# Optimization experiments

Measured on AMD Instinct MI355X. Metric: run time of the kernel, lower is better.

Reference implementation:

```python
import jax, jax.numpy as jnp
import numpy as np

N = 100000
E = 1600000
IN_CH = 128
HID = 32
HEADS = 4
OUT_CH = 32
NEG_SLOPE = 0.2


def _gat_layer(x, W, a_src, a_dst, b, src, dst, heads, out_ch):
    """PyG-style GATConv (concat=True). x: [N, F_in]; returns [N, heads*out_ch]."""
    n = x.shape[0]
    h = (x @ W).reshape(n, heads, out_ch)                    # [N, H, C]
    alpha_s = jnp.einsum('nhc,hc->nh', h, a_src)             # [N, H]
    alpha_d = jnp.einsum('nhc,hc->nh', h, a_dst)             # [N, H]
    logits = jax.nn.leaky_relu(alpha_s[src] + alpha_d[dst], NEG_SLOPE)  # [E, H]
    # segment softmax over destination node
    m = jax.ops.segment_max(logits, dst, num_segments=n)
    m = jnp.where(jnp.isfinite(m), m, 0.0)
    p = jnp.exp(logits - m[dst])
    denom = jax.ops.segment_sum(p, dst, num_segments=n)
    alpha = p / (denom[dst] + 1e-16)                         # [E, H]
    msg = h[src] * alpha[..., None]                          # [E, H, C]
    out = jax.ops.segment_sum(msg, dst, num_segments=n)      # [N, H, C]
    return out.reshape(n, heads * out_ch) + b


def setup_inputs() -> dict:
    key = jax.random.key(0)
    ks = jax.random.split(key, 16)
    x = jax.random.normal(ks[0], (N, IN_CH), dtype=jnp.float32)
    edge_index = jax.random.randint(ks[1], (2, E), 0, N, dtype=jnp.int32)

    def glorot(k, shape):
        fan = shape[0] + shape[-1]
        return jax.random.normal(k, shape, dtype=jnp.float32) * np.sqrt(2.0 / fan)

    hid = HID * HEADS  # 128
    return {
        'x': x,
        'edge_index': edge_index,
        'W1': glorot(ks[2], (IN_CH, hid)),
        'a_src1': glorot(ks[3], (HEADS, HID)),
        'a_dst1': glorot(ks[4], (HEADS, HID)),
        'b1': jnp.zeros((hid,), jnp.float32),
        'W2': glorot(ks[5], (hid, hid)),
        'a_src2': glorot(ks[6], (HEADS, HID)),
        'a_dst2': glorot(ks[7], (HEADS, HID)),
        'b2': jnp.zeros((hid,), jnp.float32),
        'W3': glorot(ks[8], (hid, OUT_CH)),
        'a_src3': glorot(ks[9], (1, OUT_CH)),
        'a_dst3': glorot(ks[10], (1, OUT_CH)),
        'b3': jnp.zeros((OUT_CH,), jnp.float32),
    }


def reference(x, edge_index, W1, a_src1, a_dst1, b1, W2, a_src2, a_dst2, b2,
              W3, a_src3, a_dst3, b3):
    # add self-loops (PyG GATConv default add_self_loops=True)
    loop = jnp.arange(N, dtype=edge_index.dtype)
    src = jnp.concatenate([edge_index[0], loop])
    dst = jnp.concatenate([edge_index[1], loop])

    h = _gat_layer(x, W1, a_src1, a_dst1, b1, src, dst, HEADS, HID)
    h = jax.nn.elu(h)
    h = _gat_layer(h, W2, a_src2, a_dst2, b2, src, dst, HEADS, HID)
    h = jax.nn.elu(h)
    out = _gat_layer(h, W3, a_src3, a_dst3, b3, src, dst, 1, OUT_CH)
    return out
```

## Files before the change

kernel.cpp:

```cpp
#include <hip/hip_runtime.h>
#include <cstdint>

#define NN 100000
#define EE 1600000
#define ET (EE + NN)
#define NBUCK 782
#define BCAP 3584

typedef unsigned int u32;
typedef unsigned short u16;
typedef short bf16x8 __attribute__((ext_vector_type(8)));
typedef float f32x4 __attribute__((ext_vector_type(4)));

__device__ __forceinline__ u16 f2bf(float f) {
    union { float f; u32 i; } v; v.f = f;
    u32 r = v.i + 0x7FFFu + ((v.i >> 16) & 1u);
    return (u16)(r >> 16);
}
__device__ __forceinline__ float bf2f(u32 u) {
    union { u32 i; float f; } v; v.i = u << 16; return v.f;
}
__device__ __forceinline__ void get_edge(const int* __restrict__ ei, int e, int& s, int& d) {
    if (e < EE) { s = ei[e]; d = ei[EE + e]; }
    else { s = e - EE; d = s; }
}
__device__ __forceinline__ float leaky(float x) { return x > 0.f ? x : 0.2f * x; }

__global__ __launch_bounds__(256) void wprep_kernel(
    const float* __restrict__ W1, const float* __restrict__ W2, const float* __restrict__ W3,
    u16* __restrict__ wt1, u16* __restrict__ wt2, u16* __restrict__ wt3)
{
    int i = blockIdx.x * 256 + threadIdx.x;
    if (i < 16384)      { int c = i >> 7, k = i & 127; wt1[i] = f2bf(W1[k * 128 + c]); }
    else if (i < 32768) { int j = i - 16384; int c = j >> 7, k = j & 127; wt2[j] = f2bf(W2[k * 128 + c]); }
    else if (i < 36864) { int j = i - 32768; int c = j >> 7, k = j & 127; wt3[j] = f2bf(W3[k * 32 + c]); }
}

template<int OUTC, bool IN16>
__global__ __launch_bounds__(256) void gemm_mfma(
    const void* __restrict__ Xv, const u16* __restrict__ Wt16g,
    const float* __restrict__ asw, const float* __restrict__ adw,
    u16* __restrict__ Hout16, float* __restrict__ as_o, float* __restrict__ ad_o)
{
    constexpr int NT = OUTC / 16;
    constexpr int LDSU = (OUTC == 128) ? 13056 : 6528;
    constexpr int HS = (OUTC == 128) ? 132 : 36;
    __shared__ u32 lds[LDSU];
    u32* wl = lds + 64 * 68;

    const int tid = threadIdx.x;
    const int r0 = blockIdx.x * 64;

    if (IN16) {
        const u32* Xg = (const u32*)Xv;
        for (int i = tid; i < 64 * 64; i += 256) {
            int r = i >> 6, k2 = i & 63;
            u32 v = 0;
            if (r0 + r < NN) v = Xg[(size_t)(r0 + r) * 64 + k2];
            lds[r * 68 + k2] = v;
        }
    } else {
        const float* Xf = (const float*)Xv;
        for (int i = tid; i < 64 * 64; i += 256) {
            int r = i >> 6, k2 = i & 63;
            u32 v = 0;
            if (r0 + r < NN) {
                float2 f = *(const float2*)(Xf + (size_t)(r0 + r) * 128 + k2 * 2);
                v = (u32)f2bf(f.x) | ((u32)f2bf(f.y) << 16);
            }
            lds[r * 68 + k2] = v;
        }
    }
    {
        const u32* Wg = (const u32*)Wt16g;
        for (int i = tid; i < OUTC * 64; i += 256) {
            int c = i >> 6, k2 = i & 63;
            wl[c * 68 + k2] = Wg[i];
        }
    }
    __syncthreads();

    const int w = tid >> 6, l = tid & 63;
    const int lm = l & 15, q = l >> 4;

    f32x4 acc[NT];
    #pragma unroll
    for (int T = 0; T < NT; T++)
        #pragma unroll
        for (int r = 0; r < 4; r++) acc[T][r] = 0.f;

    #pragma unroll
    for (int kc = 0; kc < 4; kc++) {
        bf16x8 af = *(const bf16x8*)&lds[(16 * w + lm) * 68 + kc * 16 + q * 4];
        #pragma unroll
        for (int T = 0; T < NT; T++) {
            bf16x8 bfr = *(const bf16x8*)&wl[(16 * T + lm) * 68 + kc * 16 + q * 4];
            acc[T] = __builtin_amdgcn_mfma_f32_16x16x32_bf16(af, bfr, acc[T], 0, 0, 0);
        }
    }
    __syncthreads();

    float* hl = (float*)lds;
    #pragma unroll
    for (int T = 0; T < NT; T++)
        #pragma unroll
        for (int rg = 0; rg < 4; rg++)
            hl[(16 * w + q * 4 + rg) * HS + 16 * T + lm] = acc[T][rg];
    __syncthreads();

    for (int i = tid; i < 64 * (OUTC / 2); i += 256) {
        int r = i / (OUTC / 2), k2 = i % (OUTC / 2);
        int row = r0 + r;
        if (row < NN) {
            float a = hl[r * HS + k2 * 2];
            float b = hl[r * HS + k2 * 2 + 1];
            ((u32*)Hout16)[(size_t)row * (OUTC / 2) + k2] = (u32)f2bf(a) | ((u32)f2bf(b) << 16);
        }
    }
    if (OUTC == 128) {
        const int row = tid >> 2, part = tid & 3;
        const float* hp = &hl[row * HS + part * 32];
        const float* aw = asw + part * 32;
        const float* dw = adw + part * 32;
        float s = 0.f, d = 0.f;
        #pragma unroll
        for (int c = 0; c < 32; c++) { float hv = hp[c]; s += hv * aw[c]; d += hv * dw[c]; }
        const int grow = r0 + row;
        if (grow < NN) { as_o[(size_t)grow * 4 + part] = s; ad_o[(size_t)grow * 4 + part] = d; }
    } else {
        if (tid < 64) {
            const float* hp = &hl[tid * HS];
            float s = 0.f, d = 0.f;
            #pragma unroll
            for (int c = 0; c < 32; c++) { float hv = hp[c]; s += hv * asw[c]; d += hv * adw[c]; }
            const int grow = r0 + tid;
            if (grow < NN) { as_o[grow] = s; ad_o[grow] = d; }
        }
    }
}

__global__ __launch_bounds__(256) void bin_fill_kernel(const int* __restrict__ ei,
    int* __restrict__ gcur, u32* __restrict__ pairs)
{
    __shared__ int hist[NBUCK];
    __shared__ int base[NBUCK];
    const int t = threadIdx.x;
    for (int i = t; i < NBUCK; i += 256) hist[i] = 0;
    __syncthreads();
    const int chunk = (ET + gridDim.x - 1) / gridDim.x;
    const int e0 = blockIdx.x * chunk;
    const int e1 = min(e0 + chunk, ET);
    for (int e = e0 + t; e < e1; e += 256) {
        int s, d; get_edge(ei, e, s, d);
        atomicAdd(&hist[d >> 7], 1);
    }
    __syncthreads();
    for (int i = t; i < NBUCK; i += 256) {
        int c = hist[i];
        base[i] = c ? atomicAdd(&gcur[i], c) : 0;
        hist[i] = 0;
    }
    __syncthreads();
    for (int e = e0 + t; e < e1; e += 256) {
        int s, d; get_edge(ei, e, s, d);
        int b = d >> 7;
        int pos = atomicAdd(&hist[b], 1);
        pairs[(size_t)b * BCAP + base[b] + pos] = ((u32)(d & 127) << 25) | (u32)s;
    }
}

__global__ __launch_bounds__(1024) void bscan_kernel(const int* __restrict__ bcnt,
    int* __restrict__ bbase, int* __restrict__ rowp)
{
    __shared__ int lds[1024];
    const int t = threadIdx.x;
    int v = (t < NBUCK) ? bcnt[t] : 0;
    lds[t] = v;
    __syncthreads();
    for (int off = 1; off < 1024; off <<= 1) {
        int x = (t >= off) ? lds[t - off] : 0;
        __syncthreads();
        lds[t] += x;
        __syncthreads();
    }
    if (t < NBUCK) bbase[t] = lds[t] - v;
    if (t == 0) { bbase[NBUCK] = ET; rowp[NN] = ET; }
}

__global__ __launch_bounds__(256) void bucket_csr_kernel(const u32* __restrict__ pairs,
    const int* __restrict__ bcnt, const int* __restrict__ bbase,
    int* __restrict__ rowp, int* __restrict__ col)
{
    __shared__ int hist[128], scn[128];
    __shared__ int col_lds[BCAP];
    const int b = blockIdx.x;
    const int cbase = bbase[b];
    const int cnt = bcnt[b];
    const u32* pk0 = pairs + (size_t)b * BCAP;
    const int t = threadIdx.x;
    if (t < 128) hist[t] = 0;
    __syncthreads();
    for (int i = t; i < cnt; i += 256)
        atomicAdd(&hist[pk0[i] >> 25], 1);
    __syncthreads();
    if (t < 128) scn[t] = hist[t];
    __syncthreads();
    for (int off = 1; off < 128; off <<= 1) {
        int x = (t < 128 && t >= off) ? scn[t - off] : 0;
        __syncthreads();
        if (t < 128) scn[t] += x;
        __syncthreads();
    }
    if (t < 128) {
        int ex = scn[t] - hist[t];
        int node = b * 128 + t;
        if (node < NN) rowp[node] = cbase + ex;
        hist[t] = ex;
    }
    __syncthreads();
    for (int i = t; i < cnt; i += 256) {
        u32 pk = pk0[i];
        int pos = atomicAdd(&hist[pk >> 25], 1);
        if (pos < BCAP) col_lds[pos] = pk & 0x1FFFFFFu;
    }
    __syncthreads();
    for (int i = t; i < cnt; i += 256)
        col[cbase + i] = col_lds[i];
}

template<bool DOELU>
__global__ __launch_bounds__(256) void agg4_kernel(
    const int* __restrict__ rowp, const int* __restrict__ col,
    const float* __restrict__ as_, const float* __restrict__ ad_,
    const u16* __restrict__ Hb16, const float* __restrict__ bias,
    u16* __restrict__ outp16)
{
    const int lane = threadIdx.x & 63;
    const int node = blockIdx.x * 4 + (threadIdx.x >> 6);
    const int sub = lane & 15;
    const int h = lane >> 4;

    const int start = rowp[node];
    const int end   = rowp[node + 1];
    const float adv = ad_[(size_t)node * 4 + h];
    const char* hbase = (const char*)Hb16 + lane * 4;
    const float2 bv = *(const float2*)(bias + lane * 2);

    float m = -1e30f, den = 0.f, a0 = 0.f, a1 = 0.f;
    for (int j0 = start; j0 < end; j0 += 16) {
        const int j = j0 + sub;
        const bool valid = (j < end);
        const int s = valid ? col[j] : 0;
        const float lg = valid ? leaky(as_[(size_t)s * 4 + h] + adv) : -1e30f;
        float cm = lg;
        #pragma unroll
        for (int off = 8; off; off >>= 1) cm = fmaxf(cm, __shfl_xor(cm, off));
        const float mnew = fmaxf(m, cm);
        const float sc = __expf(m - mnew);
        a0 *= sc; a1 *= sc; den *= sc; m = mnew;
        const float p = valid ? __expf(lg - m) : 0.f;
        float ps = p;
        #pragma unroll
        for (int off = 8; off; off >>= 1) ps += __shfl_xor(ps, off);
        den += ps;
        const int soff = s << 8;
        int so[16]; float pi[16];
        #pragma unroll
        for (int i = 0; i < 16; i++) {
            so[i] = __shfl(soff, i);
            pi[i] = __shfl(p, (h << 4) | i);
        }
        #pragma unroll
        for (int i = 0; i < 16; i++) {
            u32 wv = *(const u32*)(hbase + so[i]);
            a0 += pi[i] * bf2f(wv & 0xffffu);
            a1 += pi[i] * bf2f(wv >> 16);
        }
    }
    const float rden = 1.f / (den + 1e-16f);
    float v0 = a0 * rden + bv.x;
    float v1 = a1 * rden + bv.y;
    if (DOELU) {
        v0 = v0 > 0.f ? v0 : (__expf(v0) - 1.f);
        v1 = v1 > 0.f ? v1 : (__expf(v1) - 1.f);
    }
    u32 pack = (u32)f2bf(v0) | ((u32)f2bf(v1) << 16);
    *(u32*)(outp16 + (size_t)node * 128 + lane * 2) = pack;
}

__global__ __launch_bounds__(256) void agg1_kernel(
    const int* __restrict__ rowp, const int* __restrict__ col,
    const float* __restrict__ as_, const float* __restrict__ ad_,
    const u16* __restrict__ Hb16, const float* __restrict__ bias,
    float* __restrict__ outp)
{
    const int t = threadIdx.x;
    const int lane = t & 31;
    const int node = blockIdx.x * 8 + (t >> 5);

    const int start = rowp[node];
    const int end   = rowp[node + 1];
    const float adv = ad_[node];
    const char* hbase = (const char*)Hb16 + lane * 2;
    const float bvv = bias[lane];

    float m = -1e30f, den = 0.f, acc = 0.f;
    for (int j0 = start; j0 < end; j0 += 32) {
        const int j = j0 + lane;
        const bool valid = (j < end);
        const int s = valid ? col[j] : 0;
        const float lg = valid ? leaky(as_[s] + adv) : -1e30f;
        float cm = lg;
        #pragma unroll
        for (int off = 16; off; off >>= 1) cm = fmaxf(cm, __shfl_xor(cm, off, 32));
        const float mnew = fmaxf(m, cm);
        const float sc = __expf(m - mnew);
        acc *= sc; den *= sc; m = mnew;
        const float p = valid ? __expf(lg - m) : 0.f;
        float ps = p;
        #pragma unroll
        for (int off = 16; off; off >>= 1) ps += __shfl_xor(ps, off, 32);
        den += ps;
        const int soff = s << 6;
        int so[32]; float pi[32];
        #pragma unroll
        for (int i = 0; i < 32; i++) {
            so[i] = __shfl(soff, i, 32);
            pi[i] = __shfl(p, i, 32);
        }
        #pragma unroll
        for (int i = 0; i < 32; i++)
            acc += pi[i] * bf2f((u32)*(const u16*)(hbase + so[i]));
    }
    outp[(size_t)node * 32 + lane] = acc / (den + 1e-16f) + bvv;
}

extern "C" void kernel_launch(void* const* d_in, const int* in_sizes, int n_in,
                              void* d_out, int out_size, void* d_ws, size_t ws_size,
                              hipStream_t stream)
{
    const float* x   = (const float*)d_in[0];
    const int*   ei  = (const int*)d_in[1];
    const float* W1  = (const float*)d_in[2];
    const float* as1 = (const float*)d_in[3];
    const float* ad1 = (const float*)d_in[4];
    const float* b1  = (const float*)d_in[5];
    const float* W2  = (const float*)d_in[6];
    const float* as2 = (const float*)d_in[7];
    const float* ad2 = (const float*)d_in[8];
    const float* b2  = (const float*)d_in[9];
    const float* W3  = (const float*)d_in[10];
    const float* as3 = (const float*)d_in[11];
    const float* ad3 = (const float*)d_in[12];
    const float* b3  = (const float*)d_in[13];
    float* outp = (float*)d_out;

    char* ws = (char*)d_ws;
    u16*   hb16  = (u16*)(ws);
    u16*   xb16  = (u16*)(ws + 25700000);
    u16*   h3b16 = (u16*)(ws + 51400000);
    float* asb   = (float*)(ws + 57900000);
    float* adb   = (float*)(ws + 59500000);
    int*   rowp  = (int*)(ws + 61100000);
    int*   col   = (int*)(ws + 61600000);
    u32*   pairs = (u32*)(ws + 68400032);
    int*   gcur  = (int*)(ws + 79700000);
    int*   bbase = (int*)(ws + 79704096);
    u16*   wt1   = (u16*)(ws + 79710000);
    u16*   wt2   = (u16*)(ws + 79750000);
    u16*   wt3   = (u16*)(ws + 79790000);

    const dim3 B(256);
    const int gG = (NN + 63) / 64;

    wprep_kernel<<<144, B, 0, stream>>>(W1, W2, W3, wt1, wt2, wt3);
    hipMemsetAsync(gcur, 0, NBUCK * 4, stream);
    bin_fill_kernel<<<256, B, 0, stream>>>(ei, gcur, pairs);
    bscan_kernel<<<1, dim3(1024), 0, stream>>>(gcur, bbase, rowp);
    bucket_csr_kernel<<<NBUCK, B, 0, stream>>>(pairs, gcur, bbase, rowp, col);

    gemm_mfma<128, false><<<gG, B, 0, stream>>>(x, wt1, as1, ad1, hb16, asb, adb);
    agg4_kernel<true><<<NN / 4, B, 0, stream>>>(rowp, col, asb, adb, hb16, b1, xb16);

    gemm_mfma<128, true><<<gG, B, 0, stream>>>(xb16, wt2, as2, ad2, hb16, asb, adb);
    agg4_kernel<true><<<NN / 4, B, 0, stream>>>(rowp, col, asb, adb, hb16, b2, xb16);

    gemm_mfma<32, true><<<gG, B, 0, stream>>>(xb16, wt3, as3, ad3, h3b16, asb, adb);
    agg1_kernel<<<NN / 8, B, 0, stream>>>(rowp, col, asb, adb, h3b16, b3, outp);
}
```

Baseline: 454.3 us.

## Replace shuffle broadcasts with DPP reductions, LDS staging, readlane and exp2

The GEMM now stores attention logits pre-scaled by log2(e), so the aggregation kernels can use exp2f instead of __expf. The 16-lane max and sum reductions use DPP row rotations instead of xor shuffles. The per-edge weight broadcast moves from ds_bpermute shuffles into a per-wave LDS buffer read back as vectors, and source offsets are broadcast with readlane. The goal is to cut cross-lane instruction overhead in the gather loops. It relies on wave-local LDS ordering enforced only by a waitcnt, with no barrier.

Measured after the change: 473.8 us. 4.3% more time.

```diff
diff --git a/kernel.cpp b/kernel.cpp
--- a/kernel.cpp
+++ b/kernel.cpp
@@ -6,11 +6,13 @@
 #define ET (EE + NN)
 #define NBUCK 782
 #define BCAP 3584
+#define LOG2E 1.4426950408889634f
 
 typedef unsigned int u32;
 typedef unsigned short u16;
 typedef short bf16x8 __attribute__((ext_vector_type(8)));
 typedef float f32x4 __attribute__((ext_vector_type(4)));
+typedef int i32x4 __attribute__((ext_vector_type(4)));
 
 __device__ __forceinline__ u16 f2bf(float f) {
     union { float f; u32 i; } v; v.f = f;
@@ -25,6 +27,22 @@
     else { s = e - EE; d = s; }
 }
 __device__ __forceinline__ float leaky(float x) { return x > 0.f ? x : 0.2f * x; }
+
+#define DPP_ROR_F(x, CTRL) __int_as_float(__builtin_amdgcn_update_dpp(0, __float_as_int(x), (CTRL), 0xF, 0xF, true))
+__device__ __forceinline__ float rmax16(float x) {
+    x = fmaxf(x, DPP_ROR_F(x, 0x121));
+    x = fmaxf(x, DPP_ROR_F(x, 0x122));
+    x = fmaxf(x, DPP_ROR_F(x, 0x124));
+    x = fmaxf(x, DPP_ROR_F(x, 0x128));
+    return x;
+}
+__device__ __forceinline__ float rsum16(float x) {
+    x += DPP_ROR_F(x, 0x121);
+    x += DPP_ROR_F(x, 0x122);
+    x += DPP_ROR_F(x, 0x124);
+    x += DPP_ROR_F(x, 0x128);
+    return x;
+}
 
 __global__ __launch_bounds__(256) void wprep_kernel(
     const float* __restrict__ W1, const float* __restrict__ W2, const float* __restrict__ W3,
@@ -126,7 +144,10 @@
         #pragma unroll
         for (int c = 0; c < 32; c++) { float hv = hp[c]; s += hv * aw[c]; d += hv * dw[c]; }
         const int grow = r0 + row;
-        if (grow < NN) { as_o[(size_t)grow * 4 + part] = s; ad_o[(size_t)grow * 4 + part] = d; }
+        if (grow < NN) {
+            as_o[(size_t)grow * 4 + part] = s * LOG2E;
+            ad_o[(size_t)grow * 4 + part] = d * LOG2E;
+        }
     } else {
         if (tid < 64) {
             const float* hp = &hl[tid * HS];
@@ -134,7 +155,10 @@
             #pragma unroll
             for (int c = 0; c < 32; c++) { float hv = hp[c]; s += hv * asw[c]; d += hv * adw[c]; }
             const int grow = r0 + tid;
-            if (grow < NN) { as_o[grow] = s; ad_o[grow] = d; }
+            if (grow < NN) {
+                as_o[grow] = s * LOG2E;
+                ad_o[grow] = d * LOG2E;
+            }
         }
     }
 }
@@ -235,15 +259,18 @@
     const u16* __restrict__ Hb16, const float* __restrict__ bias,
     u16* __restrict__ outp16)
 {
-    const int lane = threadIdx.x & 63;
-    const int node = blockIdx.x * 4 + (threadIdx.x >> 6);
+    __shared__ float pst[4][64];
+    const int tid = threadIdx.x;
+    const int w = tid >> 6;
+    const int lane = tid & 63;
+    const int node = blockIdx.x * 4 + w;
     const int sub = lane & 15;
     const int h = lane >> 4;
 
     const int start = rowp[node];
     const int end   = rowp[node + 1];
     const float adv = ad_[(size_t)node * 4 + h];
-    const char* hbase = (const char*)Hb16 + lane * 4;
+    const int lane4 = lane << 2;
     const float2 bv = *(const float2*)(bias + lane * 2);
 
     float m = -1e30f, den = 0.f, a0 = 0.f, a1 = 0.f;
@@ -252,29 +279,27 @@
         const bool valid = (j < end);
         const int s = valid ? col[j] : 0;
         const float lg = valid ? leaky(as_[(size_t)s * 4 + h] + adv) : -1e30f;
-        float cm = lg;
-        #pragma unroll
-        for (int off = 8; off; off >>= 1) cm = fmaxf(cm, __shfl_xor(cm, off));
+        const float cm = rmax16(lg);
         const float mnew = fmaxf(m, cm);
-        const float sc = __expf(m - mnew);
+        const float sc = exp2f(m - mnew);
         a0 *= sc; a1 *= sc; den *= sc; m = mnew;
-        const float p = valid ? __expf(lg - m) : 0.f;
-        float ps = p;
-        #pragma unroll
-        for (int off = 8; off; off >>= 1) ps += __shfl_xor(ps, off);
-        den += ps;
-        const int soff = s << 8;
-        int so[16]; float pi[16];
+        const float p = valid ? exp2f(lg - m) : 0.f;
+        pst[w][lane] = p;
+        den += rsum16(p);
+        const u32 soff = (u32)s << 8;
+        asm volatile("s_waitcnt lgkmcnt(0)" ::: "memory");
+        const f32x4 pv0 = *(const f32x4*)&pst[w][h * 16 + 0];
+        const f32x4 pv1 = *(const f32x4*)&pst[w][h * 16 + 4];
+        const f32x4 pv2 = *(const f32x4*)&pst[w][h * 16 + 8];
+        const f32x4 pv3 = *(const f32x4*)&pst[w][h * 16 + 12];
         #pragma unroll
         for (int i = 0; i < 16; i++) {
-            so[i] = __shfl(soff, i);
-            pi[i] = __shfl(p, (h << 4) | i);
-        }
-        #pragma unroll
-        for (int i = 0; i < 16; i++) {
-            u32 wv = *(const u32*)(hbase + so[i]);
-            a0 += pi[i] * bf2f(wv & 0xffffu);
-            a1 += pi[i] * bf2f(wv >> 16);
+            const int so = __builtin_amdgcn_readlane((int)soff, i);
+            const char* rp = (const char*)Hb16 + so;
+            const u32 wv = *(const u32*)(rp + lane4);
+            const float pi = (i < 4 ? pv0 : i < 8 ? pv1 : i < 12 ? pv2 : pv3)[i & 3];
+            a0 += pi * bf2f(wv & 0xffffu);
+            a1 += pi * bf2f(wv >> 16);
         }
     }
     const float rden = 1.f / (den + 1e-16f);
@@ -294,45 +319,61 @@
     const u16* __restrict__ Hb16, const float* __restrict__ bias,
     float* __restrict__ outp)
 {
+    __shared__ float pst[4][64];
+    __shared__ int   sst[4][64];
     const int t = threadIdx.x;
-    const int lane = t & 31;
+    const int w = t >> 6;
+    const int lane = t & 63;
+    const int l32 = lane & 31;
+    const int half = lane >> 5;
     const int node = blockIdx.x * 8 + (t >> 5);
 
     const int start = rowp[node];
     const int end   = rowp[node + 1];
     const float adv = ad_[node];
-    const char* hbase = (const char*)Hb16 + lane * 2;
-    const float bvv = bias[lane];
+    const char* hb = (const char*)Hb16;
+    const int l2 = l32 << 1;
+    const float bvv = bias[l32];
 
     float m = -1e30f, den = 0.f, acc = 0.f;
     for (int j0 = start; j0 < end; j0 += 32) {
-        const int j = j0 + lane;
+        const int j = j0 + l32;
         const bool valid = (j < end);
         const int s = valid ? col[j] : 0;
         const float lg = valid ? leaky(as_[s] + adv) : -1e30f;
-        float cm = lg;
-        #pragma unroll
-        for (int off = 16; off; off >>= 1) cm = fmaxf(cm, __shfl_xor(cm, off, 32));
+        float cm = rmax16(lg);
+        cm = fmaxf(cm, __shfl_xor(cm, 16, 32));
         const float mnew = fmaxf(m, cm);
-        const float sc = __expf(m - mnew);
+        const float sc = exp2f(m - mnew);
         acc *= sc; den *= sc; m = mnew;
-        const float p = valid ? __expf(lg - m) : 0.f;
-        float ps = p;
-        #pragma unroll
-        for (int off = 16; off; off >>= 1) ps += __shfl_xor(ps, off, 32);
+        const float p = valid ? exp2f(lg - m) : 0.f;
+        pst[w][lane] = p;
+        sst[w][lane] = s << 6;
+        float ps = rsum16(p);
+        ps += __shfl_xor(ps, 16, 32);
         den += ps;
-        const int soff = s << 6;
-        int so[32]; float pi[32];
-        #pragma unroll
-        for (int i = 0; i < 32; i++) {
-            so[i] = __shfl(soff, i, 32);
-            pi[i] = __shfl(p, i, 32);
-        }
-        #pragma unroll
-        for (int i = 0; i < 32; i++)
-            acc += pi[i] * bf2f((u32)*(const u16*)(hbase + so[i]));
-    }
-    outp[(size_t)node * 32 + lane] = acc / (den + 1e-16f) + bvv;
+        asm volatile("s_waitcnt lgkmcnt(0)" ::: "memory");
+        const float* pb = &pst[w][half << 5];
+        const int*   sb = &sst[w][half << 5];
+        #pragma unroll
+        for (int cch = 0; cch < 2; cch++) {
+            const f32x4 pv0 = *(const f32x4*)(pb + cch * 16 + 0);
+            const f32x4 pv1 = *(const f32x4*)(pb + cch * 16 + 4);
+            const f32x4 pv2 = *(const f32x4*)(pb + cch * 16 + 8);
+            const f32x4 pv3 = *(const f32x4*)(pb + cch * 16 + 12);
+            const i32x4 sv0 = *(const i32x4*)(sb + cch * 16 + 0);
+            const i32x4 sv1 = *(const i32x4*)(sb + cch * 16 + 4);
+            const i32x4 sv2 = *(const i32x4*)(sb + cch * 16 + 8);
+            const i32x4 sv3 = *(const i32x4*)(sb + cch * 16 + 12);
+            #pragma unroll
+            for (int i = 0; i < 16; i++) {
+                const int so = (i < 4 ? sv0 : i < 8 ? sv1 : i < 12 ? sv2 : sv3)[i & 3];
+                const float pi = (i < 4 ? pv0 : i < 8 ? pv1 : i < 12 ? pv2 : pv3)[i & 3];
+                acc += pi * bf2f((u32)*(const u16*)(hb + so + l2));
+            }
+        }
+    }
+    outp[(size_t)node * 32 + l32] = acc / (den + 1e-16f) + bvv;
 }
 
 extern "C" void kernel_launch(void* const* d_in, const int* in_sizes, int n_in,
```
